# Kernel optimization log

Measured on AMD Instinct MI355X. Metric: run time of the kernel, lower is better.

The kernel has to match this reference:

```python
import jax, jax.numpy as jnp
import numpy as np

EPS = 1e-12  # torch F.normalize eps

def _normalize(x):
    n = jnp.sqrt(jnp.sum(x * x, axis=-1, keepdims=True))
    return x / jnp.maximum(n, EPS)

def bgs_extended(d6s):
    # d6s: [B, N, D, 3, 2] -> rotation [B, N, D, 3, 3] (columns b1,b2,b3)
    b1 = _normalize(d6s[..., :, 0])
    a2 = d6s[..., :, 1]
    dot = jnp.sum(b1 * a2, axis=-1, keepdims=True)
    b2 = _normalize(a2 - dot * b1)
    b3 = jnp.cross(b1, b2, axis=-1)
    return jnp.stack([b1, b2, b3], axis=-1)

def setup_inputs() -> dict:
    key = jax.random.key(0)
    k1, k2, k3, k4, k5 = jax.random.split(key, 5)
    B, N, D, F = 8, 8192, 64, 64
    X = jax.random.normal(k1, (B, N, D, 3), dtype=jnp.float32)
    J = jax.random.normal(k2, (B, N, D, 3, 2), dtype=jnp.float32)
    A = jax.random.normal(k3, (F, D), dtype=jnp.float32)
    Bm = jax.random.normal(k4, (F, D), dtype=jnp.float32)
    C = jax.random.normal(k5, (F, D), dtype=jnp.float32)
    return {"X": X, "J": J, "A": A, "Bm": Bm, "C": C}

def reference(X, J, A, Bm, C):
    R = bgs_extended(J)  # [B,N,D,3,3]
    # RT_i X = dot(column i of R, X) -> compute all three at once: [B,N,D,3]
    RTX = jnp.einsum('bndki,bndk->bndi', R, X)
    rt0, rt1, rt2 = RTX[..., 0:1], RTX[..., 1:2], RTX[..., 2:3]
    # get_rrtx(i, R, s) == R[..., :, i] * s
    a_term = R[..., :, 0] * rt0 + R[..., :, 1] * rt1
    b_term = R[..., :, 1] * rt0 - R[..., :, 0] * rt1
    c_term = R[..., :, 2] * rt2
    Y = (jnp.einsum('fe,bnei->bnfi', A, a_term)
         + jnp.einsum('fe,bnei->bnfi', Bm, b_term)
         + jnp.einsum('fe,bnei->bnfi', C, c_term))
    return Y
```

## Files before the change

### kernel.cpp

```cpp
#include <hip/hip_runtime.h>

typedef __bf16 bf16;
typedef bf16 bf16x8 __attribute__((ext_vector_type(8)));
typedef float f32x4 __attribute__((ext_vector_type(4)));

#define PTS 16
#define WPITCH 200
#define TPITCH 200


__global__ __launch_bounds__(256, 2)
void affine_linear_fused(const float* __restrict__ X, const float* __restrict__ J,
                         const float* __restrict__ A, const float* __restrict__ Bm,
                         const float* __restrict__ C, float* __restrict__ Y)
{
    __shared__ __attribute__((aligned(16))) bf16 W_lds[64 * WPITCH];
    __shared__ __attribute__((aligned(16))) bf16 T_lds[48 * TPITCH];
    __shared__ __attribute__((aligned(16))) float Y_lds[PTS * 192];

    const int tid  = threadIdx.x;
    const int wave = tid >> 6;
    const int lane = tid & 63;
    const long bn0 = (long)blockIdx.x * PTS;

    for (int idx = tid; idx < 4096; idx += 256) {
        int f = idx >> 6, d = idx & 63;
        bf16* row = &W_lds[f * WPITCH];
        row[d]       = (bf16)A[idx];
        row[64 + d]  = (bf16)Bm[idx];
        row[128 + d] = (bf16)C[idx];
    }

    for (int q = 0; q < 4; ++q) {
        int p = wave * 4 + q;
        long bn = bn0 + p;
        const float* Jc = J + (bn * 64 + lane) * 6;
        const float* Xc = X + (bn * 64 + lane) * 3;
        float a1x = Jc[0], a2x = Jc[1];
        float a1y = Jc[2], a2y = Jc[3];
        float a1z = Jc[4], a2z = Jc[5];
        float xx = Xc[0], xy = Xc[1], xz = Xc[2];

        float n1   = sqrtf(a1x*a1x + a1y*a1y + a1z*a1z);
        float inv1 = 1.0f / fmaxf(n1, 1e-12f);
        float b1x = a1x*inv1, b1y = a1y*inv1, b1z = a1z*inv1;
        float dot = b1x*a2x + b1y*a2y + b1z*a2z;
        float ux = a2x - dot*b1x, uy = a2y - dot*b1y, uz = a2z - dot*b1z;
        float n2   = sqrtf(ux*ux + uy*uy + uz*uz);
        float inv2 = 1.0f / fmaxf(n2, 1e-12f);
        float b2x = ux*inv2, b2y = uy*inv2, b2z = uz*inv2;
        float b3x = b1y*b2z - b1z*b2y;
        float b3y = b1z*b2x - b1x*b2z;
        float b3z = b1x*b2y - b1y*b2x;

        float rt0 = b1x*xx + b1y*xy + b1z*xz;
        float rt1 = b2x*xx + b2y*xy + b2z*xz;
        float rt2 = b3x*xx + b3y*xy + b3z*xz;

        float at0 = b1x*rt0 + b2x*rt1;
        float at1 = b1y*rt0 + b2y*rt1;
        float at2 = b1z*rt0 + b2z*rt1;
        float bt0 = b2x*rt0 - b1x*rt1;
        float bt1 = b2y*rt0 - b1y*rt1;
        float bt2 = b2z*rt0 - b1z*rt1;
        float ct0 = b3x*rt2, ct1 = b3y*rt2, ct2 = b3z*rt2;

        bf16* r0 = &T_lds[(p*3 + 0) * TPITCH];
        bf16* r1 = &T_lds[(p*3 + 1) * TPITCH];
        bf16* r2 = &T_lds[(p*3 + 2) * TPITCH];
        r0[lane] = (bf16)at0; r0[64+lane] = (bf16)bt0; r0[128+lane] = (bf16)ct0;
        r1[lane] = (bf16)at1; r1[64+lane] = (bf16)bt1; r1[128+lane] = (bf16)ct1;
        r2[lane] = (bf16)at2; r2[64+lane] = (bf16)bt2; r2[128+lane] = (bf16)ct2;
    }
    __syncthreads();

    const int l16 = lane & 15;
    const int lq  = lane >> 4;
    const bf16* brow = &W_lds[(wave*16 + l16) * WPITCH + lq*8];
    for (int mt = 0; mt < 3; ++mt) {
        f32x4 acc = {0.f, 0.f, 0.f, 0.f};
        const bf16* arow = &T_lds[(mt*16 + l16) * TPITCH + lq*8];
        #pragma unroll
        for (int kk = 0; kk < 6; ++kk) {
            bf16x8 af = *(const bf16x8*)(arow + kk*32);
            bf16x8 bfr = *(const bf16x8*)(brow + kk*32);
            acc = __builtin_amdgcn_mfma_f32_16x16x32_bf16(af, bfr, acc, 0, 0, 0);
        }
        int fcol = wave*16 + l16;
        #pragma unroll
        for (int r = 0; r < 4; ++r) {
            int m = mt*16 + lq*4 + r;
            int p = m / 3, i = m - p*3;
            Y_lds[p*192 + fcol*3 + i] = acc[r];
        }
    }
    __syncthreads();

    const f32x4* Ysrc = (const f32x4*)Y_lds;
    f32x4* Ydst = (f32x4*)(Y + bn0 * 192);
    #pragma unroll
    for (int idx = tid; idx < PTS*192/4; idx += 256) {
        Ydst[idx] = Ysrc[idx];
    }
}

extern "C" void kernel_launch(void* const* d_in, const int* in_sizes, int n_in,
                              void* d_out, int out_size, void* d_ws, size_t ws_size,
                              hipStream_t stream) {
    const float* X  = (const float*)d_in[0];
    const float* J  = (const float*)d_in[1];
    const float* A  = (const float*)d_in[2];
    const float* Bm = (const float*)d_in[3];
    const float* C  = (const float*)d_in[4];
    float* Y = (float*)d_out;

    const int points = in_sizes[0] / (64 * 3);
    const int blocks = points / PTS;
    affine_linear_fused<<<blocks, 256, 0, stream>>>(X, J, A, Bm, C, Y);
}
```

Measured before the change: 232.8 us.

## Load weight fragments into registers, alias Y staging onto T LDS, raise occupancy

Each wave now loads its A/Bm/C weight fragments straight from global memory into registers as bf16 MFMA operands, so the weight LDS buffer and its fill loop go away. The output staging buffer reuses the T_lds storage after an extra barrier. Together these cut the LDS footprint enough to raise the launch bound to 4 blocks per CU. All J/X loads are issued up front as float2 loads to expose more memory parallelism. The cost is higher register pressure and one more __syncthreads.

New measurement: 203.7 us. 1.14x faster.

```diff
diff --git a/kernel.cpp b/kernel.cpp
--- a/kernel.cpp
+++ b/kernel.cpp
@@ -5,41 +5,59 @@
 typedef float f32x4 __attribute__((ext_vector_type(4)));
 
 #define PTS 16
-#define WPITCH 200
 #define TPITCH 200
 
 
-__global__ __launch_bounds__(256, 2)
+__global__ __launch_bounds__(256, 4)
 void affine_linear_fused(const float* __restrict__ X, const float* __restrict__ J,
                          const float* __restrict__ A, const float* __restrict__ Bm,
                          const float* __restrict__ C, float* __restrict__ Y)
 {
-    __shared__ __attribute__((aligned(16))) bf16 W_lds[64 * WPITCH];
     __shared__ __attribute__((aligned(16))) bf16 T_lds[48 * TPITCH];
-    __shared__ __attribute__((aligned(16))) float Y_lds[PTS * 192];
 
     const int tid  = threadIdx.x;
     const int wave = tid >> 6;
     const int lane = tid & 63;
+    const int l16  = lane & 15;
+    const int lq   = lane >> 4;
     const long bn0 = (long)blockIdx.x * PTS;
 
-    for (int idx = tid; idx < 4096; idx += 256) {
-        int f = idx >> 6, d = idx & 63;
-        bf16* row = &W_lds[f * WPITCH];
-        row[d]       = (bf16)A[idx];
-        row[64 + d]  = (bf16)Bm[idx];
-        row[128 + d] = (bf16)C[idx];
+    const int f = wave * 16 + l16;
+    bf16x8 wfrag[6];
+    #pragma unroll
+    for (int kk = 0; kk < 6; ++kk) {
+        const float* src = (kk < 2) ? A : (kk < 4) ? Bm : C;
+        const f32x4* p4 = (const f32x4*)(src + f * 64 + (kk & 1) * 32 + lq * 8);
+        f32x4 lo = p4[0], hi = p4[1];
+        bf16x8 w;
+        w[0] = (bf16)lo[0]; w[1] = (bf16)lo[1]; w[2] = (bf16)lo[2]; w[3] = (bf16)lo[3];
+        w[4] = (bf16)hi[0]; w[5] = (bf16)hi[1]; w[6] = (bf16)hi[2]; w[7] = (bf16)hi[3];
+        wfrag[kk] = w;
     }
 
+    float j0[4], j1[4], j2[4], j3[4], j4[4], j5[4];
+    float x0[4], x1[4], x2[4];
+    #pragma unroll
+    for (int q = 0; q < 4; ++q) {
+        long bn = bn0 + wave * 4 + q;
+        const float* Jc = J + (bn * 64 + lane) * 6;
+        const float* Xc = X + (bn * 64 + lane) * 3;
+        float2 ja = *(const float2*)(Jc + 0);
+        float2 jb = *(const float2*)(Jc + 2);
+        float2 jc = *(const float2*)(Jc + 4);
+        j0[q] = ja.x; j1[q] = ja.y;
+        j2[q] = jb.x; j3[q] = jb.y;
+        j4[q] = jc.x; j5[q] = jc.y;
+        x0[q] = Xc[0]; x1[q] = Xc[1]; x2[q] = Xc[2];
+    }
+
+    #pragma unroll
     for (int q = 0; q < 4; ++q) {
         int p = wave * 4 + q;
-        long bn = bn0 + p;
-        const float* Jc = J + (bn * 64 + lane) * 6;
-        const float* Xc = X + (bn * 64 + lane) * 3;
-        float a1x = Jc[0], a2x = Jc[1];
-        float a1y = Jc[2], a2y = Jc[3];
-        float a1z = Jc[4], a2z = Jc[5];
-        float xx = Xc[0], xy = Xc[1], xz = Xc[2];
+        float a1x = j0[q], a2x = j1[q];
+        float a1y = j2[q], a2y = j3[q];
+        float a1z = j4[q], a2z = j5[q];
+        float xx = x0[q], xy = x1[q], xz = x2[q];
 
         float n1   = sqrtf(a1x*a1x + a1y*a1y + a1z*a1z);
         float inv1 = 1.0f / fmaxf(n1, 1e-12f);
@@ -74,24 +92,28 @@
     }
     __syncthreads();
 
-    const int l16 = lane & 15;
-    const int lq  = lane >> 4;
-    const bf16* brow = &W_lds[(wave*16 + l16) * WPITCH + lq*8];
+    f32x4 acc[3];
+    #pragma unroll
     for (int mt = 0; mt < 3; ++mt) {
-        f32x4 acc = {0.f, 0.f, 0.f, 0.f};
+        f32x4 a = {0.f, 0.f, 0.f, 0.f};
         const bf16* arow = &T_lds[(mt*16 + l16) * TPITCH + lq*8];
         #pragma unroll
         for (int kk = 0; kk < 6; ++kk) {
             bf16x8 af = *(const bf16x8*)(arow + kk*32);
-            bf16x8 bfr = *(const bf16x8*)(brow + kk*32);
-            acc = __builtin_amdgcn_mfma_f32_16x16x32_bf16(af, bfr, acc, 0, 0, 0);
+            a = __builtin_amdgcn_mfma_f32_16x16x32_bf16(af, wfrag[kk], a, 0, 0, 0);
         }
-        int fcol = wave*16 + l16;
+        acc[mt] = a;
+    }
+    __syncthreads();
+
+    float* Y_lds = (float*)T_lds;
+    #pragma unroll
+    for (int mt = 0; mt < 3; ++mt) {
         #pragma unroll
         for (int r = 0; r < 4; ++r) {
             int m = mt*16 + lq*4 + r;
             int p = m / 3, i = m - p*3;
-            Y_lds[p*192 + fcol*3 + i] = acc[r];
+            Y_lds[p*192 + f*3 + i] = acc[mt][r];
         }
     }
     __syncthreads();
```

## Restructure kernel into per-wave tiles with register double-buffered prefetch

Applied to the files above, without the earlier changes.

Each block now handles 64 points, and each wave owns 16 points processed as 4 tiles of 4. The next tile's J and X loads are prefetched into registers while the current tile is computed, so the weight staging cost is amortized over more points and global-load latency is hidden. Weight conversion uses vectorized loads, the Y LDS staging buffer and its extra barrier are removed, and accumulators are written straight to global with 4-row padding per point. The risks are higher register pressure under a 3-blocks-per-SM launch bound and strided scalar global stores in place of coalesced vector stores.

Result: faster. 209.1 us (-10.2%).

```diff
diff --git a/kernel.cpp b/kernel.cpp
--- a/kernel.cpp
+++ b/kernel.cpp
@@ -1,106 +1,124 @@
 #include <hip/hip_runtime.h>
 
 typedef __bf16 bf16;
+typedef bf16 bf16x4 __attribute__((ext_vector_type(4)));
 typedef bf16 bf16x8 __attribute__((ext_vector_type(8)));
 typedef float f32x4 __attribute__((ext_vector_type(4)));
 
-#define PTS 16
-#define WPITCH 200
-#define TPITCH 200
+#define NT 4
 
 
-__global__ __launch_bounds__(256, 2)
+__global__ __launch_bounds__(256, 3)
 void affine_linear_fused(const float* __restrict__ X, const float* __restrict__ J,
                          const float* __restrict__ A, const float* __restrict__ Bm,
                          const float* __restrict__ C, float* __restrict__ Y)
 {
-    __shared__ __attribute__((aligned(16))) bf16 W_lds[64 * WPITCH];
-    __shared__ __attribute__((aligned(16))) bf16 T_lds[48 * TPITCH];
-    __shared__ __attribute__((aligned(16))) float Y_lds[PTS * 192];
+    __shared__ __attribute__((aligned(16))) bf16 Wl[64 * 200];
+    __shared__ __attribute__((aligned(16))) bf16 Tl[4][16 * 200];
 
     const int tid  = threadIdx.x;
     const int wave = tid >> 6;
     const int lane = tid & 63;
-    const long bn0 = (long)blockIdx.x * PTS;
+    const int l16  = lane & 15;
+    const int lq   = lane >> 4;
+    const long wp0 = (long)blockIdx.x * 64 + wave * 16;
 
-    for (int idx = tid; idx < 4096; idx += 256) {
-        int f = idx >> 6, d = idx & 63;
-        bf16* row = &W_lds[f * WPITCH];
-        row[d]       = (bf16)A[idx];
-        row[64 + d]  = (bf16)Bm[idx];
-        row[128 + d] = (bf16)C[idx];
-    }
+    float jr[2][4][6], xr[2][4][3];
+    auto issue_tile = [&](int t, int s) {
+        #pragma unroll
+        for (int q = 0; q < 4; ++q) {
+            const float* jp = J + (wp0 + t*4 + q) * 384 + lane * 6;
+            float2 j01 = *(const float2*)(jp + 0);
+            float2 j23 = *(const float2*)(jp + 2);
+            float2 j45 = *(const float2*)(jp + 4);
+            jr[s][q][0] = j01.x; jr[s][q][1] = j01.y;
+            jr[s][q][2] = j23.x; jr[s][q][3] = j23.y;
+            jr[s][q][4] = j45.x; jr[s][q][5] = j45.y;
+            const float* xp = X + (wp0 + t*4 + q) * 192 + lane * 3;
+            xr[s][q][0] = xp[0]; xr[s][q][1] = xp[1]; xr[s][q][2] = xp[2];
+        }
+    };
 
-    for (int q = 0; q < 4; ++q) {
-        int p = wave * 4 + q;
-        long bn = bn0 + p;
-        const float* Jc = J + (bn * 64 + lane) * 6;
-        const float* Xc = X + (bn * 64 + lane) * 3;
-        float a1x = Jc[0], a2x = Jc[1];
-        float a1y = Jc[2], a2y = Jc[3];
-        float a1z = Jc[4], a2z = Jc[5];
-        float xx = Xc[0], xy = Xc[1], xz = Xc[2];
+    issue_tile(0, 0);
 
-        float n1   = sqrtf(a1x*a1x + a1y*a1y + a1z*a1z);
-        float inv1 = 1.0f / fmaxf(n1, 1e-12f);
-        float b1x = a1x*inv1, b1y = a1y*inv1, b1z = a1z*inv1;
-        float dot = b1x*a2x + b1y*a2y + b1z*a2z;
-        float ux = a2x - dot*b1x, uy = a2y - dot*b1y, uz = a2z - dot*b1z;
-        float n2   = sqrtf(ux*ux + uy*uy + uz*uz);
-        float inv2 = 1.0f / fmaxf(n2, 1e-12f);
-        float b2x = ux*inv2, b2y = uy*inv2, b2z = uz*inv2;
-        float b3x = b1y*b2z - b1z*b2y;
-        float b3y = b1z*b2x - b1x*b2z;
-        float b3z = b1x*b2y - b1y*b2x;
-
-        float rt0 = b1x*xx + b1y*xy + b1z*xz;
-        float rt1 = b2x*xx + b2y*xy + b2z*xz;
-        float rt2 = b3x*xx + b3y*xy + b3z*xz;
-
-        float at0 = b1x*rt0 + b2x*rt1;
-        float at1 = b1y*rt0 + b2y*rt1;
-        float at2 = b1z*rt0 + b2z*rt1;
-        float bt0 = b2x*rt0 - b1x*rt1;
-        float bt1 = b2y*rt0 - b1y*rt1;
-        float bt2 = b2z*rt0 - b1z*rt1;
-        float ct0 = b3x*rt2, ct1 = b3y*rt2, ct2 = b3z*rt2;
-
-        bf16* r0 = &T_lds[(p*3 + 0) * TPITCH];
-        bf16* r1 = &T_lds[(p*3 + 1) * TPITCH];
-        bf16* r2 = &T_lds[(p*3 + 2) * TPITCH];
-        r0[lane] = (bf16)at0; r0[64+lane] = (bf16)bt0; r0[128+lane] = (bf16)ct0;
-        r1[lane] = (bf16)at1; r1[64+lane] = (bf16)bt1; r1[128+lane] = (bf16)ct1;
-        r2[lane] = (bf16)at2; r2[64+lane] = (bf16)bt2; r2[128+lane] = (bf16)ct2;
+    #pragma unroll
+    for (int it = 0; it < 4; ++it) {
+        int idx = tid + it * 256;
+        int f = idx >> 4, d4 = (idx & 15) * 4;
+        f32x4 va = *(const f32x4*)(A  + f*64 + d4);
+        f32x4 vb = *(const f32x4*)(Bm + f*64 + d4);
+        f32x4 vc = *(const f32x4*)(C  + f*64 + d4);
+        bf16* row = Wl + f * 200;
+        *(bf16x4*)(row +       d4) = bf16x4{(bf16)va[0],(bf16)va[1],(bf16)va[2],(bf16)va[3]};
+        *(bf16x4*)(row +  64 + d4) = bf16x4{(bf16)vb[0],(bf16)vb[1],(bf16)vb[2],(bf16)vb[3]};
+        *(bf16x4*)(row + 128 + d4) = bf16x4{(bf16)vc[0],(bf16)vc[1],(bf16)vc[2],(bf16)vc[3]};
     }
     __syncthreads();
 
-    const int l16 = lane & 15;
-    const int lq  = lane >> 4;
-    const bf16* brow = &W_lds[(wave*16 + l16) * WPITCH + lq*8];
-    for (int mt = 0; mt < 3; ++mt) {
-        f32x4 acc = {0.f, 0.f, 0.f, 0.f};
-        const bf16* arow = &T_lds[(mt*16 + l16) * TPITCH + lq*8];
+    bf16* Tw = Tl[wave];
+
+    #pragma unroll
+    for (int t = 0; t < NT; ++t) {
+        const int s = t & 1;
+        if (t + 1 < NT) issue_tile(t + 1, (t + 1) & 1);
+
         #pragma unroll
-        for (int kk = 0; kk < 6; ++kk) {
-            bf16x8 af = *(const bf16x8*)(arow + kk*32);
-            bf16x8 bfr = *(const bf16x8*)(brow + kk*32);
-            acc = __builtin_amdgcn_mfma_f32_16x16x32_bf16(af, bfr, acc, 0, 0, 0);
+        for (int q = 0; q < 4; ++q) {
+            float a1x = jr[s][q][0], a2x = jr[s][q][1];
+            float a1y = jr[s][q][2], a2y = jr[s][q][3];
+            float a1z = jr[s][q][4], a2z = jr[s][q][5];
+            float xx = xr[s][q][0], xy = xr[s][q][1], xz = xr[s][q][2];
+
+            float n1   = sqrtf(a1x*a1x + a1y*a1y + a1z*a1z);
+            float inv1 = 1.0f / fmaxf(n1, 1e-12f);
+            float b1x = a1x*inv1, b1y = a1y*inv1, b1z = a1z*inv1;
+            float dot = b1x*a2x + b1y*a2y + b1z*a2z;
+            float ux = a2x - dot*b1x, uy = a2y - dot*b1y, uz = a2z - dot*b1z;
+            float n2   = sqrtf(ux*ux + uy*uy + uz*uz);
+            float inv2 = 1.0f / fmaxf(n2, 1e-12f);
+            float b2x = ux*inv2, b2y = uy*inv2, b2z = uz*inv2;
+            float b3x = b1y*b2z - b1z*b2y;
+            float b3y = b1z*b2x - b1x*b2z;
+            float b3z = b1x*b2y - b1y*b2x;
+
+            float rt0 = b1x*xx + b1y*xy + b1z*xz;
+            float rt1 = b2x*xx + b2y*xy + b2z*xz;
+            float rt2 = b3x*xx + b3y*xy + b3z*xz;
+
+            float at0 = b1x*rt0 + b2x*rt1;
+            float at1 = b1y*rt0 + b2y*rt1;
+            float at2 = b1z*rt0 + b2z*rt1;
+            float bt0 = b2x*rt0 - b1x*rt1;
+            float bt1 = b2y*rt0 - b1y*rt1;
+            float bt2 = b2z*rt0 - b1z*rt1;
+            float ct0 = b3x*rt2, ct1 = b3y*rt2, ct2 = b3z*rt2;
+
+            bf16* r0 = Tw + (4*q + 0) * 200;
+            bf16* r1 = Tw + (4*q + 1) * 200;
+            bf16* r2 = Tw + (4*q + 2) * 200;
+            r0[lane] = (bf16)at0; r0[64+lane] = (bf16)bt0; r0[128+lane] = (bf16)ct0;
+            r1[lane] = (bf16)at1; r1[64+lane] = (bf16)bt1; r1[128+lane] = (bf16)ct1;
+            r2[lane] = (bf16)at2; r2[64+lane] = (bf16)bt2; r2[128+lane] = (bf16)ct2;
         }
-        int fcol = wave*16 + l16;
+
+        const bf16* arow = Tw + l16 * 200 + lq * 8;
+        bf16x8 af[6];
         #pragma unroll
-        for (int r = 0; r < 4; ++r) {
-            int m = mt*16 + lq*4 + r;
-            int p = m / 3, i = m - p*3;
-            Y_lds[p*192 + fcol*3 + i] = acc[r];
+        for (int kk = 0; kk < 6; ++kk) af[kk] = *(const bf16x8*)(arow + kk * 32);
+
+        float* yb = Y + (wp0 + t*4 + lq) * 192 + l16 * 3;
+        #pragma unroll
+        for (int nt = 0; nt < 4; ++nt) {
+            const bf16* wr = Wl + (nt*16 + l16) * 200 + lq * 8;
+            f32x4 acc = {0.f, 0.f, 0.f, 0.f};
+            #pragma unroll
+            for (int kk = 0; kk < 6; ++kk)
+                acc = __builtin_amdgcn_mfma_f32_16x16x32_bf16(
+                          af[kk], *(const bf16x8*)(wr + kk*32), acc, 0, 0, 0);
+            yb[nt*48 + 0] = acc[0];
+            yb[nt*48 + 1] = acc[1];
+            yb[nt*48 + 2] = acc[2];
         }
-    }
-    __syncthreads();
-
-    const f32x4* Ysrc = (const f32x4*)Y_lds;
-    f32x4* Ydst = (f32x4*)(Y + bn0 * 192);
-    #pragma unroll
-    for (int idx = tid; idx < PTS*192/4; idx += 256) {
-        Ydst[idx] = Ysrc[idx];
     }
 }
 
@@ -115,6 +133,6 @@
     float* Y = (float*)d_out;
 
     const int points = in_sizes[0] / (64 * 3);
-    const int blocks = points / PTS;
+    const int blocks = points / 64;
     affine_linear_fused<<<blocks, 256, 0, stream>>>(X, J, A, Bm, C, Y);
 }
```
